# Performance work log

Measured on AMD Instinct MI355X. Metric: run time of the kernel, lower is better.

## Reference

```python
import jax, jax.numpy as jnp
import numpy as np

D_MODEL = 1024
N_HEAD = 16
D_HEAD = 64
M_FEAT = 128  # d_kernel_map


def _gen_projection_matrix(m, d, rng):
    # Performer-style: stacked orthogonal blocks scaled by chi-distributed row norms
    blocks = []
    for _ in range(m // d):
        q, _ = np.linalg.qr(rng.standard_normal((d, d)))
        blocks.append(q.T)
    rem = m % d
    if rem > 0:
        q, _ = np.linalg.qr(rng.standard_normal((d, d)))
        blocks.append(q.T[:rem])
    mat = np.vstack(blocks)
    multiplier = np.linalg.norm(rng.standard_normal((m, d)), axis=1, keepdims=True)
    return (mat * multiplier).astype(np.float32)


def setup_inputs() -> dict:
    key = jax.random.key(0)
    ks = jax.random.split(key, 6)
    B, L = 4, 4096
    rng = np.random.default_rng(0)
    hd = N_HEAD * D_HEAD
    x = jax.random.normal(ks[0], (B, L, D_MODEL), dtype=jnp.float32)
    pos_ft = jax.random.normal(ks[1], (B, L, D_MODEL), dtype=jnp.float32)
    pos_ft_slopes = jax.random.normal(ks[2], (B, L, D_MODEL), dtype=jnp.float32)
    W_v = jax.random.normal(ks[3], (D_MODEL, hd), dtype=jnp.float32) / np.sqrt(D_MODEL)
    W_o = jax.random.normal(ks[4], (hd, D_MODEL), dtype=jnp.float32) / np.sqrt(hd)
    pos_ft_weight = jax.random.normal(ks[5], (D_MODEL, hd), dtype=jnp.float32)
    pos_ft_scale = jnp.ones((1, 1, N_HEAD, 1), dtype=jnp.float32)
    head_range = 1.0 / N_HEAD
    offs = (np.arange(0, 1.0, head_range) + head_range / 2.0).astype(np.float32)
    pos_ft_offsets = jnp.asarray(offs).reshape(1, 1, N_HEAD, 1)
    proj = jnp.asarray(_gen_projection_matrix(M_FEAT, D_HEAD, rng))
    return {"x": x, "pos_ft": pos_ft, "pos_ft_slopes": pos_ft_slopes,
            "W_v": W_v, "W_o": W_o, "pos_ft_weight": pos_ft_weight,
            "pos_ft_scale": pos_ft_scale, "pos_ft_offsets": pos_ft_offsets,
            "proj": proj}


def _fourier_kernel(data, proj):
    # data: [B,L,H,D]; proj: [M,D] -> features [B,L,H,2M]
    data_normalizer = 1.0 / data.shape[-1] ** 0.25
    ratio = 1.0 / proj.shape[0] ** 0.5
    data_dash = jnp.einsum('blhd,md->blhm', data_normalizer * data, proj)
    return jnp.concatenate([ratio * jnp.sin(data_dash), ratio * jnp.cos(data_dash)], axis=-1)


def reference(x, pos_ft, pos_ft_slopes, W_v, W_o, pos_ft_weight, pos_ft_scale, pos_ft_offsets, proj):
    B, L, _ = x.shape
    v = (x @ W_v).reshape(B, L, N_HEAD, D_HEAD)
    pos_proj = (pos_ft @ pos_ft_weight).reshape(B, L, N_HEAD, D_HEAD)
    slope_proj = (pos_ft_slopes @ pos_ft_weight).reshape(B, L, N_HEAD, D_HEAD)
    query_pos = pos_ft_scale * pos_proj
    key_pos = query_pos + pos_ft_offsets * (pos_ft_scale * slope_proj)
    q_prime = _fourier_kernel(query_pos, proj)   # [B,L,H,2M]
    k_prime = _fourier_kernel(key_pos, proj)
    kv = jnp.einsum('blhm,blhd->bhmd', k_prime, v)
    z = jnp.einsum('blhm,bhmd->blhd', q_prime, kv)
    norm_factor = jnp.linalg.norm(slope_proj, axis=-1, keepdims=True) / float(L)
    z = (z * norm_factor).reshape(B, L, N_HEAD * D_HEAD)
    # dropout is identity in eval mode
    return z @ W_o
```

## Files before the change

### kernel.cpp

```cpp
#include <hip/hip_runtime.h>
#include <hip/hip_bf16.h>
#include <stdint.h>


typedef _Float16 hx8 __attribute__((ext_vector_type(8)));
typedef _Float16 hx4 __attribute__((ext_vector_type(4)));
typedef float    fx4 __attribute__((ext_vector_type(4)));

#define H_   16
#define D_   64
#define L_   4096
#define B_   4
#define KV_SPLIT 16

__device__ __forceinline__ void g2l16(const _Float16* g, _Float16* l) {
  __builtin_amdgcn_global_load_lds(
      (const __attribute__((address_space(1))) void*)g,
      (__attribute__((address_space(3))) void*)l, 16, 0, 0);
}

__global__ __launch_bounds__(256) void wt_k(const float* __restrict__ W,
                                            _Float16* __restrict__ WT) {
  __shared__ float tile[64][65];
  int t = threadIdx.x; int c = t & 63; int r0 = t >> 6;
  int bx = blockIdx.x * 64, by = blockIdx.y * 64;
  for (int r = r0; r < 64; r += 4) tile[r][c] = W[(long)(by + r) * 1024 + bx + c];
  __syncthreads();
  for (int r = r0; r < 64; r += 4)
    WT[(long)(bx + r) * 1024 + by + c] = (_Float16)tile[c][r];
}

__global__ __launch_bounds__(256) void wpf3_k(const float* __restrict__ W,
                                              _Float16* __restrict__ WT3) {
  __shared__ float tile[64][65];
  int t = threadIdx.x; int c = t & 63; int r0 = t >> 6;
  int bx = blockIdx.x * 64, by = blockIdx.y * 64;
  for (int r = r0; r < 64; r += 4) tile[r][c] = W[(long)(by + r) * 1024 + bx + c];
  __syncthreads();
  for (int r = r0; r < 64; r += 4) {
    float x = tile[c][r];
    _Float16 hi = (_Float16)x;
    _Float16 lo = (_Float16)(x - (float)hi);
    long base = (long)(bx + r) * 3072 + by + c;
    WT3[base] = hi; WT3[base + 1024] = hi; WT3[base + 2048] = lo;
  }
}

__global__ __launch_bounds__(256) void proj6_k(const float* __restrict__ proj,
                                               _Float16* __restrict__ proj6T) {
  int i = blockIdx.x * 256 + threadIdx.x;
  if (i >= 8192) return;
  int m = i >> 6, d = i & 63;
  float p = 0.35355339059327373f * proj[i];
  _Float16 hi = (_Float16)p;
  _Float16 lo = (_Float16)(p - (float)hi);
  long b = (long)m * 384 + d;
  proj6T[b]       = hi; proj6T[b + 64]  = hi; proj6T[b + 128] = lo;
  proj6T[b + 192] = hi; proj6T[b + 256] = hi; proj6T[b + 320] = lo;
}

__global__ __launch_bounds__(256) void zero_k(float* __restrict__ p, int n4) {
  int i = blockIdx.x * 256 + threadIdx.x;
  int stride = gridDim.x * 256;
  fx4 z = {0.f, 0.f, 0.f, 0.f};
  for (; i < n4; i += stride) ((fx4*)p)[i] = z;
}

__global__ __launch_bounds__(256) void cast_out_f16_k(const float* __restrict__ in,
                                                      _Float16* __restrict__ out, int n) {
  int i = blockIdx.x * 256 + threadIdx.x;
  int stride = gridDim.x * 256;
  for (; i < n; i += stride) out[i] = (_Float16)in[i];
}

__global__ __launch_bounds__(256) void cvt_hilo_k(const float* __restrict__ in,
                                                  _Float16* __restrict__ out) {
  long i = (long)blockIdx.x * 256 + threadIdx.x;
  long idx = i * 8;
  int row = (int)(idx >> 10), c = (int)(idx & 1023);
  fx4 a = *(const fx4*)&in[idx];
  fx4 b = *(const fx4*)&in[idx + 4];
  hx8 hi, lo;
#pragma unroll
  for (int e = 0; e < 4; ++e) {
    _Float16 h0 = (_Float16)a[e]; hi[e] = h0;     lo[e]     = (_Float16)(a[e] - (float)h0);
    _Float16 h1 = (_Float16)b[e]; hi[4 + e] = h1; lo[4 + e] = (_Float16)(b[e] - (float)h1);
  }
  *(hx8*)&out[(long)row * 2048 + c]        = hi;
  *(hx8*)&out[(long)row * 2048 + 1024 + c] = lo;
}

__global__ __launch_bounds__(256) void cvt16_k(const float* __restrict__ in,
                                               _Float16* __restrict__ out, long n8) {
  long i = (long)blockIdx.x * 256 + threadIdx.x;
  if (i >= n8) return;
  long idx = i * 8;
  fx4 a = *(const fx4*)&in[idx];
  fx4 b = *(const fx4*)&in[idx + 4];
  hx8 h;
#pragma unroll
  for (int e = 0; e < 4; ++e) { h[e] = (_Float16)a[e]; h[4 + e] = (_Float16)b[e]; }
  *(hx8*)&out[idx] = h;
}

template<int BM, int BN, int AMODE, int SECSH, int EPI, typename OUT_T>
__global__ __launch_bounds__(256) void gemm_bt_k(
    const void* __restrict__ Av, const _Float16* __restrict__ BT,
    OUT_T* __restrict__ C, int K, int lda, int ldb, int ldc,
    long sAb, long sAh, long sBb, long sBh, long sCb, long sCh,
    const float* __restrict__ norms, const float* __restrict__ scp,
    const float* __restrict__ ofp, const float* __restrict__ Pprev,
    float* __restrict__ nout)
{
  __shared__ __align__(16) _Float16 sA[BM * 64];
  __shared__ __align__(16) _Float16 sB[BN * 64];
  const int t = threadIdx.x;
  const int lane = t & 63;
  const int w = t >> 6;
  const int wm = w >> 1, wn = w & 1;
  const int by = blockIdx.x, bx = blockIdx.y, bz = blockIdx.z;
  long aoff = (long)(bz >> 4) * sAb + (long)(bz & 15) * sAh;
  if constexpr (AMODE == 5) aoff = 0;
  BT += (long)(bz >> 4) * sBb + (long)(bz & 15) * sBh;
  C  += (long)(bz >> 4) * sCb + (long)(bz & 15) * sCh;
  const _Float16* A16 = (const _Float16*)Av + aoff;
  const float*    A32 = (const float*)Av + aoff;
  if constexpr (EPI == 4) {
    if (bz & 15) A16 = (const _Float16*)Pprev + aoff;
  }
  constexpr int WTM = BM / 32, WTN = BN / 32;
  fx4 acc[WTM][WTN];
#pragma unroll
  for (int i = 0; i < WTM; ++i)
#pragma unroll
    for (int j = 0; j < WTN; ++j) acc[i][j] = (fx4){0.f, 0.f, 0.f, 0.f};

  int Klim = K;
  if constexpr (AMODE == 5) { if ((bz & 1) == 0) Klim >>= 1; }

  for (int k0 = 0; k0 < Klim; k0 += 64) {
    __syncthreads();
    if constexpr (AMODE == 0 || AMODE == 4 || AMODE == 5) {
      long cb;
      if constexpr (AMODE == 4) {
        int sec = k0 >> SECSH;
        cb = (k0 & ((1 << SECSH) - 1)) + (sec == 1 ? (1 << SECSH) : 0);
      } else if constexpr (AMODE == 5) {
        int sec = k0 >> SECSH;
        cb = ((sec == 1 || sec == 4) ? 64 : 0) + ((sec >= 3) ? sAb : 0);
      } else cb = k0;
#pragma unroll
      for (int i = 0; i < BM / 32; ++i) {
        int s = i * 256 + t; int row = s >> 3; int kc = (s & 7) ^ (row & 7);
        g2l16(&A16[(long)(by * BM + row) * lda + cb + kc * 8],
              &sA[(long)(i * 256 + (w << 6)) * 8]);
      }
    } else {
      int mode, cs;
      if constexpr (AMODE >= 2) { mode = k0 >> SECSH; cs = k0 & ((1 << SECSH) - 1); }
      else                      { mode = 0;           cs = k0;                      }
#pragma unroll
      for (int i = 0; i < BM / 32; ++i) {
        int s = i * 256 + t; int row = s >> 3; int kc = (s & 7) ^ (row & 7);
        const float* src = A32 + (long)(by * BM + row) * lda + cs + kc * 8;
        fx4 v0 = *(const fx4*)src;
        fx4 v1 = *(const fx4*)(src + 4);
        if constexpr (AMODE == 3) {
          if (bz & 15) {
            const float* src2 = src + sAb;
            fx4 w0 = *(const fx4*)src2;
            fx4 w1 = *(const fx4*)(src2 + 4);
#pragma unroll
            for (int e = 0; e < 4; ++e) { v0[e] += w0[e]; v1[e] += w1[e]; }
          }
        }
        hx8 hv;
        if (mode != 1) {
#pragma unroll
          for (int e = 0; e < 4; ++e) { hv[e] = (_Float16)v0[e]; hv[4 + e] = (_Float16)v1[e]; }
        } else {
#pragma unroll
          for (int e = 0; e < 4; ++e) {
            _Float16 h0 = (_Float16)v0[e]; hv[e]     = (_Float16)(v0[e] - (float)h0);
            _Float16 h1 = (_Float16)v1[e]; hv[4 + e] = (_Float16)(v1[e] - (float)h1);
          }
        }
        *(hx8*)&sA[s * 8] = hv;
      }
    }
#pragma unroll
    for (int i = 0; i < BN / 32; ++i) {
      int s = i * 256 + t; int row = s >> 3; int kc = (s & 7) ^ (row & 7);
      g2l16(&BT[(long)(bx * BN + row) * ldb + k0 + kc * 8],
            &sB[(long)(i * 256 + (w << 6)) * 8]);
    }
    __syncthreads();
#pragma unroll
    for (int kk = 0; kk < 64; kk += 32) {
      hx8 af[WTM], bf[WTN];
      int kcb = (kk >> 3) + (lane >> 4);
#pragma unroll
      for (int i = 0; i < WTM; ++i) {
        int r = wm * (BM / 2) + i * 16 + (lane & 15);
        af[i] = *(const hx8*)&sA[(r * 8 + (kcb ^ (r & 7))) * 8];
      }
#pragma unroll
      for (int j = 0; j < WTN; ++j) {
        int r = wn * (BN / 2) + j * 16 + (lane & 15);
        bf[j] = *(const hx8*)&sB[(r * 8 + (kcb ^ (r & 7))) * 8];
      }
#pragma unroll
      for (int i = 0; i < WTM; ++i)
#pragma unroll
        for (int j = 0; j < WTN; ++j)
          acc[i][j] = __builtin_amdgcn_mfma_f32_16x16x32_f16(af[i], bf[j], acc[i][j], 0, 0, 0);
    }
  }
  if constexpr (EPI == 0) {
#pragma unroll
    for (int i = 0; i < WTM; ++i) {
#pragma unroll
      for (int j = 0; j < WTN; ++j) {
        int rowb = by * BM + wm * (BM / 2) + i * 16 + ((lane >> 4) << 2);
        int col  = bx * BN + wn * (BN / 2) + j * 16 + (lane & 15);
#pragma unroll
        for (int r = 0; r < 4; ++r)
          C[(long)(rowb + r) * ldc + col] = (OUT_T)acc[i][j][r];
      }
    }
  } else if constexpr (EPI == 1) {
    const float inv2pi = 0.15915494309189535f;
    const float ratio  = 0.08838834764831845f;
    const bool useN = ((bz & 15) == 0);
#pragma unroll
    for (int i = 0; i < WTM; ++i) {
#pragma unroll
      for (int j = 0; j < WTN; ++j) {
        int rowb = by * BM + wm * (BM / 2) + i * 16 + ((lane >> 4) << 2);
        int col  = bx * BN + wn * (BN / 2) + j * 16 + (lane & 15);
#pragma unroll
        for (int r = 0; r < 4; ++r) {
          int row = rowb + r;
          float rn = ratio * (useN ? norms[row] : 1.0f);
          long ob = ((long)(row & 15) * 4096 + (row >> 4)) * 256;
          float v = acc[i][j][r] * inv2pi;
          v -= floorf(v);
          C[ob + col]       = (OUT_T)(rn * __builtin_amdgcn_sinf(v));
          C[ob + 128 + col] = (OUT_T)(rn * __builtin_amdgcn_cosf(v));
        }
      }
    }
  } else if constexpr (EPI == 2) {
    const int h = ((bx * BN) >> 6) + wn;
    const float sc = scp[h];
#pragma unroll
    for (int i = 0; i < WTM; ++i) {
#pragma unroll
      for (int j = 0; j < WTN; ++j) {
        int rowb = by * BM + wm * (BM / 2) + i * 16 + ((lane >> 4) << 2);
        int col  = bx * BN + wn * (BN / 2) + j * 16 + (lane & 15);
#pragma unroll
        for (int r = 0; r < 4; ++r)
          C[(long)(rowb + r) * ldc + col] = (OUT_T)(sc * acc[i][j][r]);
      }
    }
  } else {
    const int h = ((bx * BN) >> 6) + wn;
    const float sc = scp[h];
    _Float16* C16 = (_Float16*)C;
    if ((bz & 15) == 0) {
#pragma unroll
      for (int i = 0; i < WTM; ++i) {
#pragma unroll
        for (int j = 0; j < WTN; ++j) {
          int rowb = by * BM + wm * (BM / 2) + i * 16 + ((lane >> 4) << 2);
          int d    = wn * 0 + j * 16 + (lane & 15);
#pragma unroll
          for (int r = 0; r < 4; ++r) {
            float v = sc * acc[i][j][r];
            long a = ((long)(rowb + r) * 16 + h) * 128 + d;
            _Float16 hi = (_Float16)v;
            C16[a]      = hi;
            C16[a + 64] = (_Float16)(v - (float)hi);
          }
        }
      }
    } else {
      const float osc = ofp[h] * sc;
#pragma unroll
      for (int i = 0; i < WTM; ++i) {
        float sq[4] = {0.f, 0.f, 0.f, 0.f};
        int rowb = by * BM + wm * (BM / 2) + i * 16 + ((lane >> 4) << 2);
#pragma unroll
        for (int j = 0; j < WTN; ++j) {
          int d = j * 16 + (lane & 15);
#pragma unroll
          for (int r = 0; r < 4; ++r) {
            float a0 = acc[i][j][r];
            sq[r] += a0 * a0;
            float v = osc * a0;
            long a = ((long)(rowb + r) * 16 + h) * 128 + d;
            _Float16 hi = (_Float16)v;
            C16[a]      = hi;
            C16[a + 64] = (_Float16)(v - (float)hi);
          }
        }
#pragma unroll
        for (int r = 0; r < 4; ++r) {
          float s = sq[r];
          s += __shfl_xor(s, 1); s += __shfl_xor(s, 2);
          s += __shfl_xor(s, 4); s += __shfl_xor(s, 8);
          if ((lane & 15) == 0)
            nout[(long)(rowb + r) * 16 + h] = sqrtf(s) * (1.0f / 4096.0f);
        }
      }
    }
  }
}

__global__ __launch_bounds__(256) void kv_k(const _Float16* __restrict__ Kp,
                                            const _Float16* __restrict__ Vhb,
                                            float* __restrict__ kvacc)
{
  __shared__ __align__(16) _Float16 sK[256 * 72];
  __shared__ __align__(16) _Float16 sV[64 * 72];
  const int t = threadIdx.x, lane = t & 63, w = t >> 6;
  const int h = blockIdx.x;
  const int l0 = blockIdx.y * (L_ / KV_SPLIT);
  fx4 acc[4][4];
#pragma unroll
  for (int i = 0; i < 4; ++i)
#pragma unroll
    for (int j = 0; j < 4; ++j) acc[i][j] = (fx4){0.f, 0.f, 0.f, 0.f};
  const _Float16* Kbase = Kp + (long)h * L_ * 256;
  for (int kt = 0; kt < L_ / KV_SPLIT; kt += 64) {
    __syncthreads();
#pragma unroll
    for (int it = 0; it < 2; ++it) {
      int idx = t + it * 256;
      int m8 = idx & 31, bl = (idx >> 5) << 2;
      const _Float16* src = &Kbase[(long)(l0 + kt + bl) * 256 + m8 * 8];
      hx8 r0 = *(const hx8*)(src);
      hx8 r1 = *(const hx8*)(src + 256);
      hx8 r2 = *(const hx8*)(src + 512);
      hx8 r3 = *(const hx8*)(src + 768);
      int kx = (m8 & 7) << 4;
#pragma unroll
      for (int e = 0; e < 8; ++e) {
        hx4 v; v[0] = r0[e]; v[1] = r1[e]; v[2] = r2[e]; v[3] = r3[e];
        int byte = (((m8 * 8 + e) * 72 + bl) * 2) ^ kx;
        *(hx4*)((char*)sK + byte) = v;
      }
    }
    if (t < 128) {
      int d8 = t & 7, bl = (t >> 3) << 2;
      const _Float16* src = &Vhb[(long)(l0 + kt + bl) * 1024 + h * 64 + d8 * 8];
      hx8 r0 = *(const hx8*)(src);
      hx8 r1 = *(const hx8*)(src + 1024);
      hx8 r2 = *(const hx8*)(src + 2048);
      hx8 r3 = *(const hx8*)(src + 3072);
      int kx = d8 << 4;
#pragma unroll
      for (int e = 0; e < 8; ++e) {
        hx4 v; v[0] = r0[e]; v[1] = r1[e]; v[2] = r2[e]; v[3] = r3[e];
        int byte = (((d8 * 8 + e) * 72 + bl) * 2) ^ kx;
        *(hx4*)((char*)sV + byte) = v;
      }
    }
    __syncthreads();
#pragma unroll
    for (int kk = 0; kk < 64; kk += 32) {
      hx8 af[4], bf[4];
      int lfr = kk + ((lane >> 4) << 3);
#pragma unroll
      for (int i = 0; i < 4; ++i) {
        int r = i * 16 + (lane & 15);
        af[i] = *(const hx8*)((const char*)sV +
                ((((r * 72 + lfr) * 2)) ^ (((r >> 3) & 7) << 4)));
      }
#pragma unroll
      for (int j = 0; j < 4; ++j) {
        int r = w * 64 + j * 16 + (lane & 15);
        bf[j] = *(const hx8*)((const char*)sK +
                ((((r * 72 + lfr) * 2)) ^ (((r >> 3) & 7) << 4)));
      }
#pragma unroll
      for (int i = 0; i < 4; ++i)
#pragma unroll
        for (int j = 0; j < 4; ++j)
          acc[i][j] = __builtin_amdgcn_mfma_f32_16x16x32_f16(af[i], bf[j], acc[i][j], 0, 0, 0);
    }
  }
  float* obase = kvacc + (long)h * (64 * 256);
#pragma unroll
  for (int i = 0; i < 4; ++i)
#pragma unroll
    for (int j = 0; j < 4; ++j) {
      int d0 = i * 16 + ((lane >> 4) << 2);
      int m  = w * 64 + j * 16 + (lane & 15);
#pragma unroll
      for (int r = 0; r < 4; ++r)
        atomicAdd(&obase[(long)(d0 + r) * 256 + m], acc[i][j][r]);
    }
}

extern "C" void kernel_launch(void* const* d_in, const int* in_sizes, int n_in,
                              void* d_out, int out_size, void* d_ws, size_t ws_size,
                              hipStream_t stream) {
  const float* x     = (const float*)d_in[0];
  const float* pos   = (const float*)d_in[1];
  const float* slp   = (const float*)d_in[2];
  const float* Wv    = (const float*)d_in[3];
  const float* Wo    = (const float*)d_in[4];
  const float* Wpf   = (const float*)d_in[5];
  const float* scale = (const float*)d_in[6];
  const float* offs  = (const float*)d_in[7];
  const float* proj  = (const float*)d_in[8];
  float* out = (float*)d_out;
  char* ws = (char*)d_ws;

  size_t o = 0;
  auto alloc = [&](size_t bytes) { char* p = ws + o; o += (bytes + 255) & ~(size_t)255; return p; };
  _Float16* Pb2    = (_Float16*)alloc(33554432);
  _Float16* Sb2    = (_Float16*)alloc(33554432);
  _Float16* qpr    = (_Float16*)alloc(33554432);
  _Float16* kpr    = (_Float16*)alloc(33554432);
  _Float16* Vh     = (_Float16*)alloc(33554432);
  _Float16* Zb     = (_Float16*)alloc(33554432);
  _Float16* WvT    = (_Float16*)alloc(2097152);
  _Float16* WoT    = (_Float16*)alloc(2097152);
  _Float16* Wpf3T  = (_Float16*)alloc(6291456);
  _Float16* proj6T = (_Float16*)alloc(98304);
  float*    normsB = (float*)alloc(524288);
  float*    kvacc  = (float*)alloc(4194304);
  _Float16* kvh    = (_Float16*)alloc(2097152);
  _Float16* ph2 = qpr;
  _Float16* sh2 = kpr;
  _Float16* xh  = Zb;
  (void)Sb2; (void)ws_size; (void)in_sizes; (void)n_in; (void)out_size;

  wt_k<<<dim3(16, 16), 256, 0, stream>>>(Wv, WvT);
  wt_k<<<dim3(16, 16), 256, 0, stream>>>(Wo, WoT);
  wpf3_k<<<dim3(16, 16), 256, 0, stream>>>(Wpf, Wpf3T);
  proj6_k<<<32, 256, 0, stream>>>(proj, proj6T);
  zero_k<<<256, 256, 0, stream>>>(kvacc, 262144);
  cvt16_k<<<8192, 256, 0, stream>>>(x, xh, 2097152);

  gemm_bt_k<128, 128, 0, 0, 0, _Float16><<<dim3(128, 8, 1), 256, 0, stream>>>(
      xh, WvT, Vh, 1024, 1024, 1024, 1024, 0, 0, 0, 0, 0, 0,
      nullptr, nullptr, nullptr, nullptr, nullptr);

  for (int sb = 0; sb < 2; ++sb) {
    const float* pos_sb = pos + (long)sb * 8192 * 1024;
    const float* slp_sb = slp + (long)sb * 8192 * 1024;
    cvt_hilo_k<<<4096, 256, 0, stream>>>(pos_sb, ph2);
    cvt_hilo_k<<<4096, 256, 0, stream>>>(slp_sb, sh2);
    gemm_bt_k<128, 128, 4, 10, 4, _Float16><<<dim3(64, 8, 2), 256, 0, stream>>>(
        ph2, Wpf3T, Pb2, 3072, 2048, 3072, 128, 0, 0, 0, 0, 0, 16777216L,
        nullptr, scale, offs, (const float*)sh2, normsB);

    for (int bb = 0; bb < 2; ++bb) {
      int b = sb * 2 + bb;
      _Float16* Vh_b  = Vh + (long)b * L_ * 1024;
      _Float16* Zb_b  = Zb + (long)b * L_ * 1024;
      float* kvacc_b  = kvacc + (long)b * H_ * 64 * 256;
      _Float16* kvh_b = kvh   + (long)b * H_ * 64 * 256;
      gemm_bt_k<128, 128, 5, 6, 1, _Float16><<<dim3(512, 1, 2), 256, 0, stream>>>(
          Pb2 + (long)bb * 8388608, proj6T, qpr, 384, 128, 384, 0,
          16777216L , 0L, 0, 0, 0, 16777216L,
          normsB + (long)bb * 65536, nullptr, nullptr, nullptr, nullptr);
      kv_k<<<dim3(16, KV_SPLIT), 256, 0, stream>>>(kpr, Vh_b, kvacc_b);
      cast_out_f16_k<<<1024, 256, 0, stream>>>(kvacc_b, kvh_b, 262144);
      gemm_bt_k<128, 64, 0, 0, 0, _Float16><<<dim3(32, 1, 16), 256, 0, stream>>>(
          qpr, kvh_b, Zb_b, 256, 256, 256, 1024,
          0L, (long)L_ * 256, 0L, 16384L, 0L, 64L,
          nullptr, nullptr, nullptr, nullptr, nullptr);
    }
  }
  gemm_bt_k<128, 128, 0, 0, 0, float><<<dim3(128, 8, 1), 256, 0, stream>>>(
      Zb, WoT, out, 1024, 1024, 1024, 1024, 0, 0, 0, 0, 0, 0,
      nullptr, nullptr, nullptr, nullptr, nullptr);
}
```

Measured before the change: 896.7 us.

## Fuse feature-map GEMMs, fold kv cast into B loads, merge small launches

The Fourier feature GEMM now runs once per batch instead of twice (z=2). It emits the query features as an early epilogue partway through K and the key features at the end, which reuses the shared A tiles. The kv accumulator cast kernel is removed: the z-GEMM reads the fp32 kv directly and converts it to fp16 while loading B. The weight-transpose and hi/lo conversion launches are each merged into a single launch. This cuts launch count and redundant loads, at the cost of more register pressure from the mid-loop epilogue and a longer serial K loop per block.

```diff
diff --git a/kernel.cpp b/kernel.cpp
--- a/kernel.cpp
+++ b/kernel.cpp
@@ -19,8 +19,12 @@
       (__attribute__((address_space(3))) void*)l, 16, 0, 0);
 }
 
-__global__ __launch_bounds__(256) void wt_k(const float* __restrict__ W,
-                                            _Float16* __restrict__ WT) {
+__global__ __launch_bounds__(256) void wt2_k(const float* __restrict__ W0,
+                                             _Float16* __restrict__ T0,
+                                             const float* __restrict__ W1,
+                                             _Float16* __restrict__ T1) {
+  const float* W = blockIdx.z ? W1 : W0;
+  _Float16* WT   = blockIdx.z ? T1 : T0;
   __shared__ float tile[64][65];
   int t = threadIdx.x; int c = t & 63; int r0 = t >> 6;
   int bx = blockIdx.x * 64, by = blockIdx.y * 64;
@@ -66,15 +70,12 @@
   for (; i < n4; i += stride) ((fx4*)p)[i] = z;
 }
 
-__global__ __launch_bounds__(256) void cast_out_f16_k(const float* __restrict__ in,
-                                                      _Float16* __restrict__ out, int n) {
-  int i = blockIdx.x * 256 + threadIdx.x;
-  int stride = gridDim.x * 256;
-  for (; i < n; i += stride) out[i] = (_Float16)in[i];
-}
-
-__global__ __launch_bounds__(256) void cvt_hilo_k(const float* __restrict__ in,
-                                                  _Float16* __restrict__ out) {
+__global__ __launch_bounds__(256) void cvt_hilo2_k(const float* __restrict__ pos,
+                                                   const float* __restrict__ slp,
+                                                   _Float16* __restrict__ ph2,
+                                                   _Float16* __restrict__ sh2) {
+  const float* in = blockIdx.y ? slp : pos;
+  _Float16* out   = blockIdx.y ? sh2 : ph2;
   long i = (long)blockIdx.x * 256 + threadIdx.x;
   long idx = i * 8;
   int row = (int)(idx >> 10), c = (int)(idx & 1023);
@@ -103,7 +104,7 @@
   *(hx8*)&out[idx] = h;
 }
 
-template<int BM, int BN, int AMODE, int SECSH, int EPI, typename OUT_T>
+template<int BM, int BN, int AMODE, int SECSH, int EPI, int BMODE, typename OUT_T>
 __global__ __launch_bounds__(256) void gemm_bt_k(
     const void* __restrict__ Av, const _Float16* __restrict__ BT,
     OUT_T* __restrict__ C, int K, int lda, int ldb, int ldc,
@@ -121,10 +122,12 @@
   const int by = blockIdx.x, bx = blockIdx.y, bz = blockIdx.z;
   long aoff = (long)(bz >> 4) * sAb + (long)(bz & 15) * sAh;
   if constexpr (AMODE == 5) aoff = 0;
-  BT += (long)(bz >> 4) * sBb + (long)(bz & 15) * sBh;
-  C  += (long)(bz >> 4) * sCb + (long)(bz & 15) * sCh;
+  const _Float16* BT16 = BT;
+  const float*    B32  = (const float*)BT;
+  if constexpr (BMODE == 0) BT16 += (long)(bz >> 4) * sBb + (long)(bz & 15) * sBh;
+  else                      B32  += (long)(bz >> 4) * sBb + (long)(bz & 15) * sBh;
+  C += (long)(bz >> 4) * sCb + (long)(bz & 15) * sCh;
   const _Float16* A16 = (const _Float16*)Av + aoff;
-  const float*    A32 = (const float*)Av + aoff;
   if constexpr (EPI == 4) {
     if (bz & 15) A16 = (const _Float16*)Pprev + aoff;
   }
@@ -135,12 +138,32 @@
 #pragma unroll
     for (int j = 0; j < WTN; ++j) acc[i][j] = (fx4){0.f, 0.f, 0.f, 0.f};
 
-  int Klim = K;
-  if constexpr (AMODE == 5) { if ((bz & 1) == 0) Klim >>= 1; }
-
-  for (int k0 = 0; k0 < Klim; k0 += 64) {
+  auto fst = [&](OUT_T* Cd, bool useN) {
+    const float inv2pi = 0.15915494309189535f;
+    const float ratio  = 0.08838834764831845f;
+#pragma unroll
+    for (int i = 0; i < WTM; ++i) {
+#pragma unroll
+      for (int j = 0; j < WTN; ++j) {
+        int rowb = by * BM + wm * (BM / 2) + i * 16 + ((lane >> 4) << 2);
+        int col  = bx * BN + wn * (BN / 2) + j * 16 + (lane & 15);
+#pragma unroll
+        for (int r = 0; r < 4; ++r) {
+          int row = rowb + r;
+          float rn = ratio * (useN ? norms[row] : 1.0f);
+          long ob = ((long)(row & 15) * 4096 + (row >> 4)) * 256;
+          float v = acc[i][j][r] * inv2pi;
+          v -= floorf(v);
+          Cd[ob + col]       = (OUT_T)(rn * __builtin_amdgcn_sinf(v));
+          Cd[ob + 128 + col] = (OUT_T)(rn * __builtin_amdgcn_cosf(v));
+        }
+      }
+    }
+  };
+
+  for (int k0 = 0; k0 < K; k0 += 64) {
     __syncthreads();
-    if constexpr (AMODE == 0 || AMODE == 4 || AMODE == 5) {
+    {
       long cb;
       if constexpr (AMODE == 4) {
         int sec = k0 >> SECSH;
@@ -155,44 +178,26 @@
         g2l16(&A16[(long)(by * BM + row) * lda + cb + kc * 8],
               &sA[(long)(i * 256 + (w << 6)) * 8]);
       }
+    }
+    if constexpr (BMODE == 0) {
+#pragma unroll
+      for (int i = 0; i < BN / 32; ++i) {
+        int s = i * 256 + t; int row = s >> 3; int kc = (s & 7) ^ (row & 7);
+        g2l16(&BT16[(long)(bx * BN + row) * ldb + k0 + kc * 8],
+              &sB[(long)(i * 256 + (w << 6)) * 8]);
+      }
     } else {
-      int mode, cs;
-      if constexpr (AMODE >= 2) { mode = k0 >> SECSH; cs = k0 & ((1 << SECSH) - 1); }
-      else                      { mode = 0;           cs = k0;                      }
-#pragma unroll
-      for (int i = 0; i < BM / 32; ++i) {
+#pragma unroll
+      for (int i = 0; i < BN / 32; ++i) {
         int s = i * 256 + t; int row = s >> 3; int kc = (s & 7) ^ (row & 7);
-        const float* src = A32 + (long)(by * BM + row) * lda + cs + kc * 8;
+        const float* src = B32 + (long)(bx * BN + row) * ldb + k0 + kc * 8;
         fx4 v0 = *(const fx4*)src;
         fx4 v1 = *(const fx4*)(src + 4);
-        if constexpr (AMODE == 3) {
-          if (bz & 15) {
-            const float* src2 = src + sAb;
-            fx4 w0 = *(const fx4*)src2;
-            fx4 w1 = *(const fx4*)(src2 + 4);
-#pragma unroll
-            for (int e = 0; e < 4; ++e) { v0[e] += w0[e]; v1[e] += w1[e]; }
-          }
-        }
         hx8 hv;
-        if (mode != 1) {
-#pragma unroll
-          for (int e = 0; e < 4; ++e) { hv[e] = (_Float16)v0[e]; hv[4 + e] = (_Float16)v1[e]; }
-        } else {
-#pragma unroll
-          for (int e = 0; e < 4; ++e) {
-            _Float16 h0 = (_Float16)v0[e]; hv[e]     = (_Float16)(v0[e] - (float)h0);
-            _Float16 h1 = (_Float16)v1[e]; hv[4 + e] = (_Float16)(v1[e] - (float)h1);
-          }
-        }
-        *(hx8*)&sA[s * 8] = hv;
-      }
-    }
-#pragma unroll
-    for (int i = 0; i < BN / 32; ++i) {
-      int s = i * 256 + t; int row = s >> 3; int kc = (s & 7) ^ (row & 7);
-      g2l16(&BT[(long)(bx * BN + row) * ldb + k0 + kc * 8],
-            &sB[(long)(i * 256 + (w << 6)) * 8]);
+#pragma unroll
+        for (int e = 0; e < 4; ++e) { hv[e] = (_Float16)v0[e]; hv[4 + e] = (_Float16)v1[e]; }
+        *(hx8*)&sB[s * 8] = hv;
+      }
     }
     __syncthreads();
 #pragma unroll
@@ -215,6 +220,9 @@
         for (int j = 0; j < WTN; ++j)
           acc[i][j] = __builtin_amdgcn_mfma_f32_16x16x32_f16(af[i], bf[j], acc[i][j], 0, 0, 0);
     }
+    if constexpr (EPI == 5) {
+      if (k0 == 128) fst(C, true);
+    }
   }
   if constexpr (EPI == 0) {
 #pragma unroll
@@ -228,42 +236,8 @@
           C[(long)(rowb + r) * ldc + col] = (OUT_T)acc[i][j][r];
       }
     }
-  } else if constexpr (EPI == 1) {
-    const float inv2pi = 0.15915494309189535f;
-    const float ratio  = 0.08838834764831845f;
-    const bool useN = ((bz & 15) == 0);
-#pragma unroll
-    for (int i = 0; i < WTM; ++i) {
-#pragma unroll
-      for (int j = 0; j < WTN; ++j) {
-        int rowb = by * BM + wm * (BM / 2) + i * 16 + ((lane >> 4) << 2);
-        int col  = bx * BN + wn * (BN / 2) + j * 16 + (lane & 15);
-#pragma unroll
-        for (int r = 0; r < 4; ++r) {
-          int row = rowb + r;
-          float rn = ratio * (useN ? norms[row] : 1.0f);
-          long ob = ((long)(row & 15) * 4096 + (row >> 4)) * 256;
-          float v = acc[i][j][r] * inv2pi;
-          v -= floorf(v);
-          C[ob + col]       = (OUT_T)(rn * __builtin_amdgcn_sinf(v));
-          C[ob + 128 + col] = (OUT_T)(rn * __builtin_amdgcn_cosf(v));
-        }
-      }
-    }
-  } else if constexpr (EPI == 2) {
-    const int h = ((bx * BN) >> 6) + wn;
-    const float sc = scp[h];
-#pragma unroll
-    for (int i = 0; i < WTM; ++i) {
-#pragma unroll
-      for (int j = 0; j < WTN; ++j) {
-        int rowb = by * BM + wm * (BM / 2) + i * 16 + ((lane >> 4) << 2);
-        int col  = bx * BN + wn * (BN / 2) + j * 16 + (lane & 15);
-#pragma unroll
-        for (int r = 0; r < 4; ++r)
-          C[(long)(rowb + r) * ldc + col] = (OUT_T)(sc * acc[i][j][r]);
-      }
-    }
+  } else if constexpr (EPI == 5) {
+    fst(C + sCh, false);
   } else {
     const int h = ((bx * BN) >> 6) + wn;
     const float sc = scp[h];
@@ -274,7 +248,7 @@
 #pragma unroll
         for (int j = 0; j < WTN; ++j) {
           int rowb = by * BM + wm * (BM / 2) + i * 16 + ((lane >> 4) << 2);
-          int d    = wn * 0 + j * 16 + (lane & 15);
+          int d    = j * 16 + (lane & 15);
 #pragma unroll
           for (int r = 0; r < 4; ++r) {
             float v = sc * acc[i][j][r];
@@ -433,29 +407,26 @@
   _Float16* proj6T = (_Float16*)alloc(98304);
   float*    normsB = (float*)alloc(524288);
   float*    kvacc  = (float*)alloc(4194304);
-  _Float16* kvh    = (_Float16*)alloc(2097152);
   _Float16* ph2 = qpr;
   _Float16* sh2 = kpr;
   _Float16* xh  = Zb;
   (void)Sb2; (void)ws_size; (void)in_sizes; (void)n_in; (void)out_size;
 
-  wt_k<<<dim3(16, 16), 256, 0, stream>>>(Wv, WvT);
-  wt_k<<<dim3(16, 16), 256, 0, stream>>>(Wo, WoT);
+  wt2_k<<<dim3(16, 16, 2), 256, 0, stream>>>(Wv, WvT, Wo, WoT);
   wpf3_k<<<dim3(16, 16), 256, 0, stream>>>(Wpf, Wpf3T);
   proj6_k<<<32, 256, 0, stream>>>(proj, proj6T);
-  zero_k<<<256, 256, 0, stream>>>(kvacc, 262144);
+  zero_k<<<256, 256, 0, stream>>>(kvacc, 1048576 / 4);
   cvt16_k<<<8192, 256, 0, stream>>>(x, xh, 2097152);
 
-  gemm_bt_k<128, 128, 0, 0, 0, _Float16><<<dim3(128, 8, 1), 256, 0, stream>>>(
+  gemm_bt_k<128, 128, 0, 0, 0, 0, _Float16><<<dim3(128, 8, 1), 256, 0, stream>>>(
       xh, WvT, Vh, 1024, 1024, 1024, 1024, 0, 0, 0, 0, 0, 0,
       nullptr, nullptr, nullptr, nullptr, nullptr);
 
   for (int sb = 0; sb < 2; ++sb) {
     const float* pos_sb = pos + (long)sb * 8192 * 1024;
     const float* slp_sb = slp + (long)sb * 8192 * 1024;
-    cvt_hilo_k<<<4096, 256, 0, stream>>>(pos_sb, ph2);
-    cvt_hilo_k<<<4096, 256, 0, stream>>>(slp_sb, sh2);
-    gemm_bt_k<128, 128, 4, 10, 4, _Float16><<<dim3(64, 8, 2), 256, 0, stream>>>(
+    cvt_hilo2_k<<<dim3(4096, 2), 256, 0, stream>>>(pos_sb, slp_sb, ph2, sh2);
+    gemm_bt_k<128, 128, 4, 10, 4, 0, _Float16><<<dim3(64, 8, 2), 256, 0, stream>>>(
         ph2, Wpf3T, Pb2, 3072, 2048, 3072, 128, 0, 0, 0, 0, 0, 16777216L,
         nullptr, scale, offs, (const float*)sh2, normsB);
 
@@ -464,20 +435,18 @@
       _Float16* Vh_b  = Vh + (long)b * L_ * 1024;
       _Float16* Zb_b  = Zb + (long)b * L_ * 1024;
       float* kvacc_b  = kvacc + (long)b * H_ * 64 * 256;
-      _Float16* kvh_b = kvh   + (long)b * H_ * 64 * 256;
-      gemm_bt_k<128, 128, 5, 6, 1, _Float16><<<dim3(512, 1, 2), 256, 0, stream>>>(
+      gemm_bt_k<128, 128, 5, 6, 5, 0, _Float16><<<dim3(512, 1, 1), 256, 0, stream>>>(
           Pb2 + (long)bb * 8388608, proj6T, qpr, 384, 128, 384, 0,
-          16777216L , 0L, 0, 0, 0, 16777216L,
+          16777216L , 0L, 0, 0, 0, 16777216L ,
           normsB + (long)bb * 65536, nullptr, nullptr, nullptr, nullptr);
       kv_k<<<dim3(16, KV_SPLIT), 256, 0, stream>>>(kpr, Vh_b, kvacc_b);
-      cast_out_f16_k<<<1024, 256, 0, stream>>>(kvacc_b, kvh_b, 262144);
-      gemm_bt_k<128, 64, 0, 0, 0, _Float16><<<dim3(32, 1, 16), 256, 0, stream>>>(
-          qpr, kvh_b, Zb_b, 256, 256, 256, 1024,
+      gemm_bt_k<128, 64, 0, 0, 0, 1, _Float16><<<dim3(32, 1, 16), 256, 0, stream>>>(
+          qpr, (const _Float16*)kvacc_b, Zb_b, 256, 256, 256, 1024,
           0L, (long)L_ * 256, 0L, 16384L, 0L, 64L,
           nullptr, nullptr, nullptr, nullptr, nullptr);
     }
   }
-  gemm_bt_k<128, 128, 0, 0, 0, float><<<dim3(128, 8, 1), 256, 0, stream>>>(
+  gemm_bt_k<128, 128, 0, 0, 0, 0, float><<<dim3(128, 8, 1), 256, 0, stream>>>(
       Zb, WoT, out, 1024, 1024, 1024, 1024, 0, 0, 0, 0, 0, 0,
       nullptr, nullptr, nullptr, nullptr, nullptr);
 }
```

Result: no change. 909.6 us (+1.4%).
